# Kernel optimization log

Measured on AMD Instinct MI355X. Metric: run time of the kernel, lower is better.

## Reference

```python
import jax, jax.numpy as jnp
import numpy as np

P, L, H = 3, 4, 6          # window size, num scales, num heads
EPS = 1e-5                 # LayerNorm eps (PyTorch default)


def setup_inputs() -> dict:
    key = jax.random.key(0)
    B, T, D = 8, 4096, 768
    ks = jax.random.split(key, 12)
    s = 0.02
    w = lambda k, shape: (jax.random.normal(k, shape, jnp.float32) * s)
    z = lambda n: jnp.zeros((n,), jnp.float32)
    return {
        "x": jax.random.normal(ks[0], (B, T, D), jnp.float32),
        "ln_g": jnp.ones((D,), jnp.float32),
        "ln_b": z(D),
        "qw": w(ks[1], (D, D)), "qb": z(D),
        "kw": w(ks[2], (D, D)), "kb": z(D),
        "vw": w(ks[3], (D, D)), "vb": z(D),
        "inw": w(ks[4], (3 * D, D)), "inb": z(3 * D),   # MHA in_proj
        "mow": w(ks[5], (D, D)), "mob": z(D),            # MHA out_proj
        "ow": w(ks[6], (D, D)), "ob": z(D),              # output_proj
    }


def _layernorm(x, g, b):
    mu = jnp.mean(x, -1, keepdims=True)
    var = jnp.mean((x - mu) ** 2, -1, keepdims=True)
    return (x - mu) * jax.lax.rsqrt(var + EPS) * g + b


def _mha_windows(q, k, v, inw, inb, mow, mob):
    # q,k,v: [B, W, P, D] -- batched tiny attention over all windows at once
    B, W, Pw, D = q.shape
    hd = D // H
    wq, wk, wv = inw[:D], inw[D:2 * D], inw[2 * D:]
    bq, bk, bv = inb[:D], inb[D:2 * D], inb[2 * D:]
    qp = (q @ wq.T + bq).reshape(B, W, Pw, H, hd)
    kp = (k @ wk.T + bk).reshape(B, W, Pw, H, hd)
    vp = (v @ wv.T + bv).reshape(B, W, Pw, H, hd)
    scores = jnp.einsum('bwqhd,bwkhd->bwhqk', qp, kp) / jnp.sqrt(jnp.float32(hd))
    attn = jax.nn.softmax(scores, axis=-1)
    o = jnp.einsum('bwhqk,bwkhd->bwqhd', attn, vp).reshape(B, W, Pw, D)
    return o @ mow.T + mob


def reference(x, ln_g, ln_b, qw, qb, kw, kb, vw, vb, inw, inb, mow, mob, ow, ob):
    B, T, D = x.shape
    xn = _layernorm(x, ln_g, ln_b)
    Q = xn @ qw.T + qb
    K = xn @ kw.T + kb
    V = xn @ vw.T + vb
    acc = jnp.zeros_like(x)
    for kk in range(L):
        scale = P ** kk
        if T < scale:
            continue
        Lp = T // scale
        pool = lambda z: z[:, :Lp * scale].reshape(B, Lp, scale, D).mean(axis=2)
        pQ, pK, pV = pool(Q), pool(K), pool(V)
        W = Lp // P
        if W == 0:
            continue
        win = lambda z: z[:, :W * P].reshape(B, W, P, D)
        o = _mha_windows(win(pQ), win(pK), win(pV), inw, inb, mow, mob)
        so = o.reshape(B, W * P, D)                       # concat of windows
        idx = (jnp.arange(T) * (W * P)) // T              # nearest interp to T
        up = so[:, idx]
        acc = acc + jax.nn.gelu(up, approximate=False)    # exact GELU (torch default)
    out = acc @ ow.T + ob
    return x + out
```

## Files before the change

kernel.cpp:

```cpp
#include <hip/hip_runtime.h>
#include <stdint.h>

typedef short s16x8 __attribute__((ext_vector_type(8)));
typedef float f32x4 __attribute__((ext_vector_type(4)));

__device__ __forceinline__ unsigned short f2bf(float f) {
  unsigned u = __builtin_bit_cast(unsigned, f);
  u = (u + 0x7FFFu + ((u >> 16) & 1u)) >> 16;
  return (unsigned short)u;
}
__device__ __forceinline__ float bf2f(unsigned short h) {
  unsigned u = ((unsigned)h) << 16;
  return __builtin_bit_cast(float, u);
}

__device__ __forceinline__ void gload_lds16(const void* g, void* l) {
  __builtin_amdgcn_global_load_lds((__attribute__((address_space(1))) void*)g,
                                   (__attribute__((address_space(3))) void*)l,
                                   16, 0, 0);
}

__global__ __launch_bounds__(256)
void mstr_convw(const float* __restrict__ inw, const float* __restrict__ mow,
                const float* __restrict__ ow, unsigned short* __restrict__ inwB,
                unsigned short* __restrict__ mowB, unsigned short* __restrict__ owB)
{
  long i = (long)blockIdx.x * 256 + threadIdx.x;
  const long n1 = 589824;
  if (i < 3 * n1)      inwB[i] = f2bf(inw[i]);
  else if (i < 4 * n1) mowB[i - 3 * n1] = f2bf(mow[i - 3 * n1]);
  else                 owB[i - 4 * n1] = f2bf(ow[i - 4 * n1]);
}

__global__ __launch_bounds__(256)
void mstr_transpose(const float* __restrict__ qw, const float* __restrict__ kw,
                    const float* __restrict__ vw, unsigned short* __restrict__ wT)
{
  const float* src = (blockIdx.z == 0) ? qw : (blockIdx.z == 1) ? kw : vw;
  unsigned short* dst = wT + (long)blockIdx.z * 589824;
  __shared__ float tile[32][33];
  int tx = threadIdx.x & 31, ty = threadIdx.x >> 5;
  int j0 = blockIdx.x * 32, k0 = blockIdx.y * 32;
#pragma unroll
  for (int i = 0; i < 4; ++i)
    tile[ty + i * 8][tx] = src[(long)(j0 + ty + i * 8) * 768 + k0 + tx];
  __syncthreads();
#pragma unroll
  for (int i = 0; i < 4; ++i)
    dst[(long)(k0 + ty + i * 8) * 768 + j0 + tx] = f2bf(tile[tx][ty + i * 8]);
}

__global__ __launch_bounds__(256)
void mstr_biascomb(const float* __restrict__ inw, const float* __restrict__ inb,
                   const float* __restrict__ qb, const float* __restrict__ kb,
                   const float* __restrict__ vb, float* __restrict__ bc,
                   float* __restrict__ zb)
{
  int gid = blockIdx.x * 256 + threadIdx.x;
  if (gid < 768) zb[gid] = 0.f;
  int s = gid / 768, c = gid - s * 768;
  const float* b = (s == 0) ? qb : (s == 1) ? kb : vb;
  const float* wrow = inw + (long)(s * 768 + c) * 768;
  float a = inb[s * 768 + c];
  for (int j = 0; j < 768; ++j) a += b[j] * wrow[j];
  bc[gid] = a;
}

__global__ __launch_bounds__(256)
void mstr_ln(const float* __restrict__ x, const float* __restrict__ g,
             const float* __restrict__ bt, unsigned short* __restrict__ xn)
{
  int blk = blockIdx.x;
  int bb = blk / 4095, t = blk - bb * 4095;
  const float* xr = x + ((long)bb * 4096 + t) * 768;
  unsigned short* orow = xn + (long)blk * 768;
  int tid = threadIdx.x;
  float v0 = xr[tid], v1 = xr[tid + 256], v2 = xr[tid + 512];
  float s = v0 + v1 + v2;
  float s2 = v0 * v0 + v1 * v1 + v2 * v2;
#pragma unroll
  for (int o = 32; o > 0; o >>= 1) { s += __shfl_down(s, o, 64); s2 += __shfl_down(s2, o, 64); }
  __shared__ float rs[4], rq[4];
  int lane = tid & 63, wid = tid >> 6;
  if (lane == 0) { rs[wid] = s; rq[wid] = s2; }
  __syncthreads();
  float S = rs[0] + rs[1] + rs[2] + rs[3];
  float S2 = rq[0] + rq[1] + rq[2] + rq[3];
  float mu = S * (1.0f / 768.0f);
  float var = S2 * (1.0f / 768.0f) - mu * mu;
  float rstd = rsqrtf(var + 1e-5f);
  orow[tid] = f2bf((v0 - mu) * rstd * g[tid] + bt[tid]);
  orow[tid + 256] = f2bf((v1 - mu) * rstd * g[tid + 256] + bt[tid + 256]);
  orow[tid + 512] = f2bf((v2 - mu) * rstd * g[tid + 512] + bt[tid + 512]);
}

template<int EPI>
__global__ __launch_bounds__(256)
void mstr_gemm(const unsigned short* __restrict__ A, int M,
               const unsigned short* __restrict__ W,
               const float* __restrict__ bias,
               unsigned short* __restrict__ outb,
               float* __restrict__ outf,
               const float* __restrict__ xadd,
               int rowDiv, int rowStride)
{
  __shared__ unsigned short As[128 * 32];
  __shared__ unsigned short Bs[128 * 32];
  const int tid = threadIdx.x;
  const int lane = tid & 63;
  const int wid = tid >> 6;
  const int wr = wid >> 1, wc = wid & 1;
  const long row0 = (long)blockIdx.x * 128;
  const int col0 = blockIdx.y * 128;
  const unsigned short* Bg = W + (long)col0 * 768;
  const int sr = tid >> 2;
  const int sc = (tid & 3) * 8;
  const int fr = lane & 15;
  const int fk = (lane >> 4) * 8;
  long rA0 = row0 + sr;       if (rA0 >= M) rA0 = M - 1;
  long rA1 = row0 + sr + 64;  if (rA1 >= M) rA1 = M - 1;
  const unsigned short* AgR0 = A + rA0 * 768 + sc;
  const unsigned short* AgR1 = A + rA1 * 768 + sc;
  const unsigned short* BgR0 = Bg + (long)sr * 768 + sc;
  const unsigned short* BgR1 = Bg + (long)(sr + 64) * 768 + sc;
  f32x4 acc[4][4] = {};
  for (int k0 = 0; k0 < 768; k0 += 32) {
    __syncthreads();
    gload_lds16(AgR0 + k0, (char*)As + tid * 16);
    gload_lds16(AgR1 + k0, (char*)As + 4096 + tid * 16);
    gload_lds16(BgR0 + k0, (char*)Bs + tid * 16);
    gload_lds16(BgR1 + k0, (char*)Bs + 4096 + tid * 16);
    __syncthreads();
    s16x8 af[4], bfv[4];
#pragma unroll
    for (int m = 0; m < 4; ++m)
      af[m] = *(const s16x8*)(&As[(wr * 64 + m * 16 + fr) * 32 + fk]);
#pragma unroll
    for (int n = 0; n < 4; ++n)
      bfv[n] = *(const s16x8*)(&Bs[(wc * 64 + n * 16 + fr) * 32 + fk]);
#pragma unroll
    for (int m = 0; m < 4; ++m)
#pragma unroll
      for (int n = 0; n < 4; ++n)
        acc[m][n] = __builtin_amdgcn_mfma_f32_16x16x32_bf16(af[m], bfv[n], acc[m][n], 0, 0, 0);
  }
#pragma unroll
  for (int m = 0; m < 4; ++m) {
#pragma unroll
    for (int r = 0; r < 4; ++r) {
      long gr = row0 + wr * 64 + m * 16 + (lane >> 4) * 4 + r;
      if (gr < M) {
        long orow;
        if (EPI == 0) {
          int q = (int)gr / rowDiv;
          orow = (long)q * rowStride + ((int)gr - q * rowDiv);
        } else {
          orow = gr;
        }
#pragma unroll
        for (int n = 0; n < 4; ++n) {
          int c = col0 + wc * 64 + n * 16 + (lane & 15);
          float v = acc[m][n][r] + bias[c];
          if (EPI == 0) {
            outb[orow * 768 + c] = f2bf(v);
          } else {
            long o = orow * 768 + c;
            outf[o] = v + xadd[o];
          }
        }
      }
    }
  }
}

__global__ __launch_bounds__(384)
void mstr_pool(unsigned short* qp, unsigned short* kp, unsigned short* vp,
               int srcOff, int dstOff, int Ndst)
{
  unsigned short* p = (blockIdx.y == 0) ? qp : (blockIdx.y == 1) ? kp : vp;
  int tok = blockIdx.x;
  int bb = tok / Ndst, j = tok - bb * Ndst;
  long sb = ((long)bb * 6063 + srcOff + 3 * j) * 768 + threadIdx.x * 2;
  long db = ((long)bb * 6063 + dstOff + j) * 768 + threadIdx.x * 2;
  unsigned a = *(const unsigned*)(p + sb);
  unsigned b = *(const unsigned*)(p + sb + 768);
  unsigned c = *(const unsigned*)(p + sb + 1536);
  float lo = (bf2f((unsigned short)a) + bf2f((unsigned short)b) + bf2f((unsigned short)c)) * (1.0f / 3.0f);
  float hi = (bf2f((unsigned short)(a >> 16)) + bf2f((unsigned short)(b >> 16)) + bf2f((unsigned short)(c >> 16))) * (1.0f / 3.0f);
  unsigned o = (unsigned)f2bf(lo) | ((unsigned)f2bf(hi) << 16);
  *(unsigned*)(p + db) = o;
}

__global__ __launch_bounds__(256)
void mstr_attn(unsigned short* qp, unsigned short* kp, unsigned short* vp, int nwaves)
{
  int gw = blockIdx.x * 4 + (threadIdx.x >> 6);
  if (gw >= nwaves) return;
  int lane = threadIdx.x & 63;
  int win = gw / 6, h = gw - win * 6;
  int bb = win / 2021, ww = win - bb * 2021;
  int row0;
  if (ww < 1365)      row0 = 3 * ww;
  else if (ww < 1820) row0 = 4095 + 3 * (ww - 1365);
  else if (ww < 1971) row0 = 5460 + 3 * (ww - 1820);
  else                row0 = 5913 + 3 * (ww - 1971);
  long base = ((long)bb * 6063 + row0) * 768 + h * 128 + lane * 2;
  float q[3][2], k[3][2], v[3][2];
#pragma unroll
  for (int i = 0; i < 3; ++i) {
    unsigned uq = *(const unsigned*)(qp + base + i * 768);
    unsigned uk = *(const unsigned*)(kp + base + i * 768);
    unsigned uv = *(const unsigned*)(vp + base + i * 768);
    q[i][0] = bf2f((unsigned short)uq); q[i][1] = bf2f((unsigned short)(uq >> 16));
    k[i][0] = bf2f((unsigned short)uk); k[i][1] = bf2f((unsigned short)(uk >> 16));
    v[i][0] = bf2f((unsigned short)uv); v[i][1] = bf2f((unsigned short)(uv >> 16));
  }
  float s[3][3];
#pragma unroll
  for (int i = 0; i < 3; ++i)
#pragma unroll
    for (int j = 0; j < 3; ++j)
      s[i][j] = q[i][0] * k[j][0] + q[i][1] * k[j][1];
#pragma unroll
  for (int st = 1; st < 64; st <<= 1) {
#pragma unroll
    for (int i = 0; i < 3; ++i)
#pragma unroll
      for (int j = 0; j < 3; ++j)
        s[i][j] += __shfl_xor(s[i][j], st, 64);
  }
  const float scl = 0.088388347648318447f;
#pragma unroll
  for (int i = 0; i < 3; ++i) {
    float s0 = s[i][0] * scl, s1 = s[i][1] * scl, s2 = s[i][2] * scl;
    float m = fmaxf(s0, fmaxf(s1, s2));
    float e0 = __expf(s0 - m), e1 = __expf(s1 - m), e2 = __expf(s2 - m);
    float inv = 1.0f / (e0 + e1 + e2);
    e0 *= inv; e1 *= inv; e2 *= inv;
    float o0 = e0 * v[0][0] + e1 * v[1][0] + e2 * v[2][0];
    float o1 = e0 * v[0][1] + e1 * v[1][1] + e2 * v[2][1];
    unsigned o = (unsigned)f2bf(o0) | ((unsigned)f2bf(o1) << 16);
    *(unsigned*)(qp + base + i * 768) = o;
  }
}

__global__ __launch_bounds__(256)
void mstr_gelusum(const unsigned short* __restrict__ omo, unsigned short* __restrict__ acc)
{
  long gid = (long)blockIdx.x * 256 + threadIdx.x;
  int d2 = (int)(gid % 384);
  long row = gid / 384;
  int bb = (int)(row >> 12);
  int t = (int)(row & 4095);
  const int NkA[4] = {4095, 1365, 453, 150};
  const int soA[4] = {0, 4095, 5460, 5913};
  float a0 = 0.f, a1 = 0.f;
#pragma unroll
  for (int kk = 0; kk < 4; ++kk) {
    int idx = (t * NkA[kk]) >> 12;
    long tok = (long)bb * 6063 + soA[kk] + idx;
    unsigned u = *(const unsigned*)(omo + tok * 768 + d2 * 2);
    float x0 = bf2f((unsigned short)u), x1 = bf2f((unsigned short)(u >> 16));
    a0 += 0.5f * x0 * (1.0f + erff(x0 * 0.70710678118654752f));
    a1 += 0.5f * x1 * (1.0f + erff(x1 * 0.70710678118654752f));
  }
  unsigned o = (unsigned)f2bf(a0) | ((unsigned)f2bf(a1) << 16);
  *(unsigned*)(acc + row * 768 + d2 * 2) = o;
}

extern "C" void kernel_launch(void* const* d_in, const int* in_sizes, int n_in,
                              void* d_out, int out_size, void* d_ws, size_t ws_size,
                              hipStream_t stream)
{
  const float* x   = (const float*)d_in[0];
  const float* lng = (const float*)d_in[1];
  const float* lnb = (const float*)d_in[2];
  const float* qw  = (const float*)d_in[3];
  const float* qb  = (const float*)d_in[4];
  const float* kw  = (const float*)d_in[5];
  const float* kb  = (const float*)d_in[6];
  const float* vw  = (const float*)d_in[7];
  const float* vb  = (const float*)d_in[8];
  const float* inw = (const float*)d_in[9];
  const float* inb = (const float*)d_in[10];
  const float* mob = (const float*)d_in[12];
  const float* ow  = (const float*)d_in[13];
  const float* ob  = (const float*)d_in[14];

  const long n1 = 589824;
  char* ws = (char*)d_ws;
  size_t off = 0;
  auto alloc = [&](size_t bytes) -> char* {
    char* p = ws + off;
    off += (bytes + 255) & ~(size_t)255;
    return p;
  };
  unsigned short* Wc = (unsigned short*)alloc((size_t)5 * n1 * 2);
  float* bc = (float*)alloc(2304 * 4);
  float* zb = (float*)alloc(768 * 4);
  size_t fixed = off;

  int g = 0;
  const int cands[4] = {8, 4, 2, 1};
  for (int ci = 0; ci < 4; ++ci) {
    int c = cands[ci];
    size_t need = fixed + (size_t)c * 4096 * 768 * 2
                + 2 * (size_t)c * 6063 * 768 * 2
                + 1024;
    if (need <= ws_size) { g = c; break; }
  }
  if (!g) return;

  char* GR = ws + fixed;
  unsigned short* xnacc = (unsigned short*)GR;
  unsigned short* qp = xnacc + (size_t)g * 4096 * 768;
  unsigned short* kp = qp + (size_t)g * 6063 * 768;
  unsigned short* inwB = (unsigned short*)GR;
  unsigned short* wT   = inwB + 3 * n1;

  unsigned short* mowB = Wc + 3 * n1;
  unsigned short* owB  = Wc + 4 * n1;

  mstr_convw<<<dim3(11520), dim3(256), 0, stream>>>(inw, (const float*)d_in[11], ow, inwB, mowB, owB);
  mstr_transpose<<<dim3(24, 24, 3), dim3(256), 0, stream>>>(qw, kw, vw, wT);
  mstr_biascomb<<<dim3(9), dim3(256), 0, stream>>>(inw, inb, qb, kb, vb, bc, zb);
  for (int s = 0; s < 3; ++s)
    mstr_gemm<0><<<dim3(6, 6), dim3(256), 0, stream>>>(inwB + (long)s * n1, 768, wT + (long)s * n1,
                                                       zb, Wc + (long)s * n1, nullptr, nullptr, 768, 768);

  int ng = 8 / g;
  for (int gi = 0; gi < ng; ++gi) {
    const float* xg = x + (long)gi * g * 4096 * 768;
    unsigned short* vp = (unsigned short*)d_out + (long)gi * g * 4096 * 768 * 2;
    mstr_ln<<<dim3(g * 4095), dim3(256), 0, stream>>>(xg, lng, lnb, xnacc);
    int M1 = g * 4095, gb1 = (M1 + 127) / 128;
    mstr_gemm<0><<<dim3(gb1, 6), dim3(256), 0, stream>>>(xnacc, M1, Wc + 0 * n1, bc + 0,    qp, nullptr, nullptr, 4095, 6063);
    mstr_gemm<0><<<dim3(gb1, 6), dim3(256), 0, stream>>>(xnacc, M1, Wc + 1 * n1, bc + 768,  kp, nullptr, nullptr, 4095, 6063);
    mstr_gemm<0><<<dim3(gb1, 6), dim3(256), 0, stream>>>(xnacc, M1, Wc + 2 * n1, bc + 1536, vp, nullptr, nullptr, 4095, 6063);
    mstr_pool<<<dim3(g * 1365, 3), dim3(384), 0, stream>>>(qp, kp, vp, 0, 4095, 1365);
    mstr_pool<<<dim3(g * 453, 3), dim3(384), 0, stream>>>(qp, kp, vp, 4095, 5460, 453);
    mstr_pool<<<dim3(g * 150, 3), dim3(384), 0, stream>>>(qp, kp, vp, 5460, 5913, 150);
    int nw = g * 2021 * 6;
    mstr_attn<<<dim3((nw + 3) / 4), dim3(256), 0, stream>>>(qp, kp, vp, nw);
    int M2 = g * 6063;
    mstr_gemm<0><<<dim3((M2 + 127) / 128, 6), dim3(256), 0, stream>>>(qp, M2, mowB, mob, kp, nullptr, nullptr, M2, 0);
    mstr_gelusum<<<dim3(g * 6144), dim3(256), 0, stream>>>(kp, xnacc);
    int M3 = g * 4096;
    mstr_gemm<1><<<dim3(M3 / 128, 6), dim3(256), 0, stream>>>(xnacc, M3, owB, ob, nullptr,
                                                              (float*)d_out + (long)gi * g * 4096 * 768, xg, M3, 0);
  }
}
```

Baseline: 670.1 us.

## Fuse Q/K/V projection GEMMs into one launch with XCD-aware block swizzle

Flattens the GEMM grid to 1D and remaps block IDs so consecutive tiles sharing A rows land on the same XCD, improving L2 reuse on the multi-die MI355X. The three separate Q/K/V projection launches are merged into one launch over 2304 output columns, with each block routing its output to the q, k or v buffer by column segment. This cuts launch count, gives one larger grid, and lets all three projections reuse the same activation tile from cache. It adds per-block index arithmetic and assumes the combined weight and bias buffers are laid out contiguously.

After: 628.1 us. 1.07x faster.

```diff
diff --git a/kernel.cpp b/kernel.cpp
--- a/kernel.cpp
+++ b/kernel.cpp
@@ -99,19 +99,27 @@
 void mstr_gemm(const unsigned short* __restrict__ A, int M,
                const unsigned short* __restrict__ W,
                const float* __restrict__ bias,
-               unsigned short* __restrict__ outb,
+               unsigned short* __restrict__ out0,
+               unsigned short* __restrict__ out1,
+               unsigned short* __restrict__ out2,
                float* __restrict__ outf,
                const float* __restrict__ xadd,
-               int rowDiv, int rowStride)
-{
+               int rowDiv, int rowStride, int NC, int nwg)
+{
+  int orig = blockIdx.x;
+  int swq = nwg >> 3, swr = nwg & 7;
+  int xcd = orig & 7, sidx = orig >> 3;
+  int wg = (xcd < swr ? xcd * (swq + 1) : swr * (swq + 1) + (xcd - swr) * swq) + sidx;
+  int rowp = wg / NC, colp = wg - rowp * NC;
+
   __shared__ unsigned short As[128 * 32];
   __shared__ unsigned short Bs[128 * 32];
   const int tid = threadIdx.x;
   const int lane = tid & 63;
   const int wid = tid >> 6;
   const int wr = wid >> 1, wc = wid & 1;
-  const long row0 = (long)blockIdx.x * 128;
-  const int col0 = blockIdx.y * 128;
+  const long row0 = (long)rowp * 128;
+  const int col0 = colp * 128;
   const unsigned short* Bg = W + (long)col0 * 768;
   const int sr = tid >> 2;
   const int sc = (tid & 3) * 8;
@@ -144,6 +152,9 @@
       for (int n = 0; n < 4; ++n)
         acc[m][n] = __builtin_amdgcn_mfma_f32_16x16x32_bf16(af[m], bfv[n], acc[m][n], 0, 0, 0);
   }
+  int seg = (col0 >= 1536) ? 2 : (col0 >= 768 ? 1 : 0);
+  unsigned short* outp = (seg == 0) ? out0 : (seg == 1) ? out1 : out2;
+  int csub = seg * 768;
 #pragma unroll
   for (int m = 0; m < 4; ++m) {
 #pragma unroll
@@ -152,8 +163,8 @@
       if (gr < M) {
         long orow;
         if (EPI == 0) {
-          int q = (int)gr / rowDiv;
-          orow = (long)q * rowStride + ((int)gr - q * rowDiv);
+          int qq = (int)gr / rowDiv;
+          orow = (long)qq * rowStride + ((int)gr - qq * rowDiv);
         } else {
           orow = gr;
         }
@@ -162,7 +173,7 @@
           int c = col0 + wc * 64 + n * 16 + (lane & 15);
           float v = acc[m][n][r] + bias[c];
           if (EPI == 0) {
-            outb[orow * 768 + c] = f2bf(v);
+            outp[orow * 768 + (c - csub)] = f2bf(v);
           } else {
             long o = orow * 768 + c;
             outf[o] = v + xadd[o];
@@ -325,8 +336,9 @@
   mstr_transpose<<<dim3(24, 24, 3), dim3(256), 0, stream>>>(qw, kw, vw, wT);
   mstr_biascomb<<<dim3(9), dim3(256), 0, stream>>>(inw, inb, qb, kb, vb, bc, zb);
   for (int s = 0; s < 3; ++s)
-    mstr_gemm<0><<<dim3(6, 6), dim3(256), 0, stream>>>(inwB + (long)s * n1, 768, wT + (long)s * n1,
-                                                       zb, Wc + (long)s * n1, nullptr, nullptr, 768, 768);
+    mstr_gemm<0><<<dim3(36), dim3(256), 0, stream>>>(inwB + (long)s * n1, 768, wT + (long)s * n1,
+                                                     zb, Wc + (long)s * n1, Wc + (long)s * n1,
+                                                     Wc + (long)s * n1, nullptr, nullptr, 768, 768, 6, 36);
 
   int ng = 8 / g;
   for (int gi = 0; gi < ng; ++gi) {
@@ -334,19 +346,24 @@
     unsigned short* vp = (unsigned short*)d_out + (long)gi * g * 4096 * 768 * 2;
     mstr_ln<<<dim3(g * 4095), dim3(256), 0, stream>>>(xg, lng, lnb, xnacc);
     int M1 = g * 4095, gb1 = (M1 + 127) / 128;
-    mstr_gemm<0><<<dim3(gb1, 6), dim3(256), 0, stream>>>(xnacc, M1, Wc + 0 * n1, bc + 0,    qp, nullptr, nullptr, 4095, 6063);
-    mstr_gemm<0><<<dim3(gb1, 6), dim3(256), 0, stream>>>(xnacc, M1, Wc + 1 * n1, bc + 768,  kp, nullptr, nullptr, 4095, 6063);
-    mstr_gemm<0><<<dim3(gb1, 6), dim3(256), 0, stream>>>(xnacc, M1, Wc + 2 * n1, bc + 1536, vp, nullptr, nullptr, 4095, 6063);
+    int nwg1 = gb1 * 18;
+    mstr_gemm<0><<<dim3(nwg1), dim3(256), 0, stream>>>(xnacc, M1, Wc, bc,
+                                                       qp, kp, vp, nullptr, nullptr,
+                                                       4095, 6063, 18, nwg1);
     mstr_pool<<<dim3(g * 1365, 3), dim3(384), 0, stream>>>(qp, kp, vp, 0, 4095, 1365);
     mstr_pool<<<dim3(g * 453, 3), dim3(384), 0, stream>>>(qp, kp, vp, 4095, 5460, 453);
     mstr_pool<<<dim3(g * 150, 3), dim3(384), 0, stream>>>(qp, kp, vp, 5460, 5913, 150);
     int nw = g * 2021 * 6;
     mstr_attn<<<dim3((nw + 3) / 4), dim3(256), 0, stream>>>(qp, kp, vp, nw);
     int M2 = g * 6063;
-    mstr_gemm<0><<<dim3((M2 + 127) / 128, 6), dim3(256), 0, stream>>>(qp, M2, mowB, mob, kp, nullptr, nullptr, M2, 0);
+    int nwg2 = ((M2 + 127) / 128) * 6;
+    mstr_gemm<0><<<dim3(nwg2), dim3(256), 0, stream>>>(qp, M2, mowB, mob, kp, kp, kp,
+                                                       nullptr, nullptr, M2, 0, 6, nwg2);
     mstr_gelusum<<<dim3(g * 6144), dim3(256), 0, stream>>>(kp, xnacc);
     int M3 = g * 4096;
-    mstr_gemm<1><<<dim3(M3 / 128, 6), dim3(256), 0, stream>>>(xnacc, M3, owB, ob, nullptr,
-                                                              (float*)d_out + (long)gi * g * 4096 * 768, xg, M3, 0);
-  }
-}
+    int nwg3 = (M3 / 128) * 6;
+    mstr_gemm<1><<<dim3(nwg3), dim3(256), 0, stream>>>(xnacc, M3, owB, ob, nullptr, nullptr, nullptr,
+                                                       (float*)d_out + (long)gi * g * 4096 * 768, xg,
+                                                       M3, 0, 6, nwg3);
+  }
+}
```
